# Optimization experiments

Measured on AMD Instinct MI355X. Metric: run time of the kernel, lower is better.

The kernel has to match this reference:

```python
import jax, jax.numpy as jnp
import numpy as np

N = 100000
E = 3200000
NEG_SLOPE = 0.2


def setup_inputs() -> dict:
    key = jax.random.key(0)
    ks = jax.random.split(key, 12)
    x = jax.random.normal(ks[0], (N, 4), dtype=jnp.float32)
    edge_index = jax.random.randint(ks[1], (2, E), 0, N, dtype=jnp.int64)
    # GATConv(4, 16, heads=4): lin (no bias), att_src/att_dst [H, C], bias [H*C]
    W1 = jax.random.normal(ks[2], (4, 4 * 16), dtype=jnp.float32) * 0.5
    as1 = jax.random.normal(ks[3], (4, 16), dtype=jnp.float32) * 0.5
    ad1 = jax.random.normal(ks[4], (4, 16), dtype=jnp.float32) * 0.5
    b1 = jnp.zeros((64,), dtype=jnp.float32)
    # GATConv(64, 2, heads=4)
    W2 = jax.random.normal(ks[5], (64, 4 * 2), dtype=jnp.float32) * 0.125
    as2 = jax.random.normal(ks[6], (4, 2), dtype=jnp.float32) * 0.5
    ad2 = jax.random.normal(ks[7], (4, 2), dtype=jnp.float32) * 0.5
    b2 = jnp.zeros((8,), dtype=jnp.float32)
    # out head Linear(8, 1)
    Wout = jax.random.normal(ks[8], (8, 1), dtype=jnp.float32) * 0.35
    bout = jnp.zeros((1,), dtype=jnp.float32)
    return {"x": x, "edge_index": edge_index, "W1": W1, "as1": as1, "ad1": ad1,
            "b1": b1, "W2": W2, "as2": as2, "ad2": ad2, "b2": b2,
            "Wout": Wout, "bout": bout}


def gat_conv(x, ei, W, a_src, a_dst, b, H, C, n):
    # PyG GATConv (concat=True, negative_slope=0.2), self-loops already in ei
    xw = (x @ W).reshape(n, H, C)                      # [N, H, C]
    src, dst = ei[0], ei[1]
    alpha_s = jnp.einsum('nhc,hc->nh', xw, a_src)      # [N, H]
    alpha_d = jnp.einsum('nhc,hc->nh', xw, a_dst)      # [N, H]
    e = jax.nn.leaky_relu(alpha_s[src] + alpha_d[dst], NEG_SLOPE)  # [E, H]
    # segment softmax over incoming edges of each destination node
    m = jax.ops.segment_max(e, dst, num_segments=n)    # [N, H]
    e = jnp.exp(e - m[dst])
    denom = jax.ops.segment_sum(e, dst, num_segments=n)
    alpha = e / (denom[dst] + 1e-16)                   # [E, H]
    msg = xw[src] * alpha[:, :, None]                  # [E, H, C]
    out = jax.ops.segment_sum(msg, dst, num_segments=n)  # [N, H, C]
    return out.reshape(n, H * C) + b


def reference(x, edge_index, W1, as1, ad1, b1, W2, as2, ad2, b2, Wout, bout):
    n = x.shape[0]
    ar = jnp.arange(n, dtype=edge_index.dtype)
    ei = jnp.concatenate([edge_index, jnp.stack([ar, ar])], axis=1)  # add self-loops
    h = jax.nn.elu(gat_conv(x, ei, W1, as1, ad1, b1, 4, 16, n))       # [N, 64]
    h = jax.nn.elu(gat_conv(h, ei, W2, as2, ad2, b2, 4, 2, n))        # [N, 8]
    g = jnp.mean(h, axis=0, keepdims=True)  # global_mean_pool, batch all zeros -> [1, 8]
    return jax.nn.sigmoid(g @ Wout + bout)  # [1, 1]
```

## Files before the change

kernel.cpp:

```cpp
#include <hip/hip_runtime.h>
#include <hip/hip_fp8.h>

#define NEG 0.2f
#define BSZ 224
#define MAXBUK 512
#define NBIN 512

typedef float v2f __attribute__((ext_vector_type(2)));

__device__ __forceinline__ float elufast(float x){ return x > 0.0f ? x : __expf(x) - 1.0f; }
__device__ __forceinline__ float b2f(unsigned short b){ return __uint_as_float((unsigned)b << 16); }
__device__ __forceinline__ unsigned short f2b(float x){
    unsigned u = __float_as_uint(x);
    return (unsigned short)((u + 0x7FFFu + ((u >> 16) & 1u)) >> 16);
}

__device__ __forceinline__ void fma8(uint2 r, float w, v2f* acc){
    v2f w2 = {w, w};
    v2f f0 = __builtin_amdgcn_cvt_pk_f32_fp8(r.x, false);
    v2f f1 = __builtin_amdgcn_cvt_pk_f32_fp8(r.x, true);
    v2f f2 = __builtin_amdgcn_cvt_pk_f32_fp8(r.y, false);
    v2f f3 = __builtin_amdgcn_cvt_pk_f32_fp8(r.y, true);
    acc[0] = __builtin_elementwise_fma(f0, w2, acc[0]);
    acc[1] = __builtin_elementwise_fma(f1, w2, acc[1]);
    acc[2] = __builtin_elementwise_fma(f2, w2, acc[2]);
    acc[3] = __builtin_elementwise_fma(f3, w2, acc[3]);
}

__global__ void k_l1_node(const float* __restrict__ x, const float* __restrict__ W1,
                          const float* __restrict__ as1, const float* __restrict__ ad1,
                          unsigned char* __restrict__ xw1, uint2* __restrict__ asvb,
                          float* __restrict__ adv, int N){
    __shared__ float sW[256], sA[64], sD[64];
    int tid = threadIdx.x;
    sW[tid] = W1[tid];
    if (tid < 64){ sA[tid] = as1[tid]; sD[tid] = ad1[tid]; }
    __syncthreads();
    int i = blockIdx.x * 256 + tid;
    if (i >= N) return;
    float4 xv = ((const float4*)x)[i];
    const v2f* sW0 = (const v2f*)sW;
    const v2f* sW1v = (const v2f*)(sW + 64);
    const v2f* sW2v = (const v2f*)(sW + 128);
    const v2f* sW3v = (const v2f*)(sW + 192);
    v2f xx = {xv.x, xv.x}, yy = {xv.y, xv.y}, zz = {xv.z, xv.z}, ww = {xv.w, xv.w};
    v2f xwv[32];
    #pragma unroll
    for (int j = 0; j < 32; j++){
        v2f t = xx * sW0[j];
        t = __builtin_elementwise_fma(yy, sW1v[j], t);
        t = __builtin_elementwise_fma(zz, sW2v[j], t);
        t = __builtin_elementwise_fma(ww, sW3v[j], t);
        xwv[j] = t;
    }
    unsigned wv[16];
    #pragma unroll
    for (int j = 0; j < 16; j++){
        unsigned p = 0;
        p = __builtin_amdgcn_cvt_pk_fp8_f32(xwv[2 * j].x,     xwv[2 * j].y,     p, false);
        p = __builtin_amdgcn_cvt_pk_fp8_f32(xwv[2 * j + 1].x, xwv[2 * j + 1].y, p, true);
        wv[j] = p;
    }
    uint4* dp = (uint4*)(xw1 + (size_t)i * 64);
    dp[0] = make_uint4(wv[0],  wv[1],  wv[2],  wv[3]);
    dp[1] = make_uint4(wv[4],  wv[5],  wv[6],  wv[7]);
    dp[2] = make_uint4(wv[8],  wv[9],  wv[10], wv[11]);
    dp[3] = make_uint4(wv[12], wv[13], wv[14], wv[15]);
    const v2f* sAv = (const v2f*)sA;
    const v2f* sDv = (const v2f*)sD;
    float al[4];
    #pragma unroll
    for (int h = 0; h < 4; h++){
        v2f asv = {0.f, 0.f}, adw = {0.f, 0.f};
        #pragma unroll
        for (int c2 = 0; c2 < 8; c2++){
            asv = __builtin_elementwise_fma(xwv[h * 8 + c2], sAv[h * 8 + c2], asv);
            adw = __builtin_elementwise_fma(xwv[h * 8 + c2], sDv[h * 8 + c2], adw);
        }
        al[h] = asv.x + asv.y;
        adv[i * 4 + h] = adw.x + adw.y;
    }
    asvb[i] = make_uint2((unsigned)f2b(al[0]) | ((unsigned)f2b(al[1]) << 16),
                         (unsigned)f2b(al[2]) | ((unsigned)f2b(al[3]) << 16));
}

__global__ void k_bcount(const int* __restrict__ dst, int* __restrict__ blkcnt,
                         int E, int chunksz, int nbuk){
    __shared__ int hist[MAXBUK];
    for (int b = threadIdx.x; b < nbuk; b += 256) hist[b] = 0;
    __syncthreads();
    int e0 = blockIdx.x * chunksz, e1 = min(E, e0 + chunksz);
    for (int e = e0 + threadIdx.x; e < e1; e += 256)
        atomicAdd(&hist[(unsigned)dst[e] / BSZ], 1);
    __syncthreads();
    for (int b = threadIdx.x; b < nbuk; b += 256)
        blkcnt[b * NBIN + blockIdx.x] = hist[b];
}

__global__ void k_scanA(int* __restrict__ blkcnt, int* __restrict__ btot){
    __shared__ int ts[256];
    int b = blockIdx.x, t = threadIdx.x;
    int base = b * NBIN + t * 2;
    int a0 = blkcnt[base], a1 = blkcnt[base + 1];
    int sum = a0 + a1;
    ts[t] = sum; __syncthreads();
    for (int s = 1; s < 256; s <<= 1){
        int tmp = (t >= s) ? ts[t - s] : 0;
        __syncthreads();
        ts[t] += tmp;
        __syncthreads();
    }
    int excl = ts[t] - sum;
    blkcnt[base] = excl;
    blkcnt[base + 1] = excl + a0;
    if (t == 255) btot[b] = ts[255];
}

__global__ void k_scanB(const int* __restrict__ btot, int* __restrict__ bstart, int nbuk){
    __shared__ int ts[512];
    int t = threadIdx.x;
    int v = (t < nbuk) ? btot[t] : 0;
    int orig = v;
    ts[t] = v; __syncthreads();
    for (int s = 1; s < 512; s <<= 1){
        int tmp = (t >= s) ? ts[t - s] : 0;
        __syncthreads();
        ts[t] += tmp;
        __syncthreads();
    }
    if (t < nbuk) bstart[t] = ts[t] - orig;
    if (t == 511) bstart[nbuk] = ts[511];
}

__global__ void k_bin(const int* __restrict__ src, const int* __restrict__ dst,
                      const int* __restrict__ blkcnt, const int* __restrict__ bstart,
                      unsigned* __restrict__ staged, int E, int chunksz, int nbuk){
    __shared__ int cur[MAXBUK];
    for (int b = threadIdx.x; b < nbuk; b += 256)
        cur[b] = bstart[b] + blkcnt[b * NBIN + blockIdx.x];
    __syncthreads();
    int e0 = blockIdx.x * chunksz, e1 = min(E, e0 + chunksz);
    for (int e = e0 + threadIdx.x; e < e1; e += 256){
        int d = dst[e];
        int buk = (unsigned)d / BSZ;
        int pos = atomicAdd(&cur[buk], 1);
        staged[pos] = (unsigned)src[e] | ((unsigned)(d - buk * BSZ) << 17);
    }
}

__global__ void k_local(const int* __restrict__ bstart, const unsigned* __restrict__ staged,
                        int* __restrict__ offp, int* __restrict__ csr, int N){
    __shared__ int deg[BSZ];
    __shared__ int cur[BSZ];
    __shared__ int ts[256];
    int b = blockIdx.x, t = threadIdx.x;
    int lo = b * BSZ, hi = min(N, lo + BSZ);
    int e0 = bstart[b], e1 = bstart[b + 1];
    if (t < BSZ) deg[t] = 0;
    __syncthreads();
    for (int e = e0 + t; e < e1; e += 256)
        atomicAdd(&deg[staged[e] >> 17], 1);
    __syncthreads();
    int v = (t < BSZ) ? deg[t] : 0;
    ts[t] = v; __syncthreads();
    for (int s = 1; s < 256; s <<= 1){
        int tmp = (t >= s) ? ts[t - s] : 0;
        __syncthreads();
        ts[t] += tmp;
        __syncthreads();
    }
    if (t < BSZ){
        cur[t] = e0 + ts[t] - v;
        if (lo + t < hi) offp[lo + t] = e0 + ts[t];
    }
    __syncthreads();
    for (int e = e0 + t; e < e1; e += 256){
        unsigned se = staged[e];
        int pos = atomicAdd(&cur[se >> 17], 1);
        csr[pos] = (int)(se & 0x1FFFFu);
    }
}

__global__ void k_l1_gather(const int* __restrict__ off, const int* __restrict__ csr,
                            const uint2* __restrict__ asvb, const float* __restrict__ adv,
                            const unsigned char* __restrict__ xw1, const float* __restrict__ b1,
                            unsigned char* __restrict__ h1f8, int N){
    int tid = threadIdx.x;
    int wid = (int)(((long)blockIdx.x * 256 + tid) >> 6);
    if (wid >= N) return;
    int lane = tid & 63;
    int g = lane >> 3;
    int q = lane & 7;
    int h = q >> 1;
    float advd = adv[wid * 4 + h];
    const unsigned char* xwq = xw1 + q * 8;
    const char* asvbh = (const char*)asvb + h * 2;

    v2f acc2[4] = {{0.f, 0.f}, {0.f, 0.f}, {0.f, 0.f}, {0.f, 0.f}};
    float den = 0.f;
    int k = wid ? off[wid - 1] : 0;
    int end = off[wid];
    for (; k + 32 <= end; k += 32){
        int s0 = csr[k + g];
        int s1 = csr[k + 8 + g];
        int s2 = csr[k + 16 + g];
        int s3 = csr[k + 24 + g];
        uint2 r0 = *(const uint2*)(xwq + ((size_t)s0 << 6));
        uint2 r1 = *(const uint2*)(xwq + ((size_t)s1 << 6));
        uint2 r2 = *(const uint2*)(xwq + ((size_t)s2 << 6));
        uint2 r3 = *(const uint2*)(xwq + ((size_t)s3 << 6));
        float a0 = b2f(*(const unsigned short*)(asvbh + ((size_t)s0 << 3)));
        float a1 = b2f(*(const unsigned short*)(asvbh + ((size_t)s1 << 3)));
        float a2 = b2f(*(const unsigned short*)(asvbh + ((size_t)s2 << 3)));
        float a3 = b2f(*(const unsigned short*)(asvbh + ((size_t)s3 << 3)));
        float t0 = a0 + advd, t1 = a1 + advd, t2 = a2 + advd, t3 = a3 + advd;
        float w0 = __expf(fmaxf(t0, NEG * t0));
        float w1 = __expf(fmaxf(t1, NEG * t1));
        float w2 = __expf(fmaxf(t2, NEG * t2));
        float w3 = __expf(fmaxf(t3, NEG * t3));
        den += (w0 + w1) + (w2 + w3);
        fma8(r0, w0, acc2);
        fma8(r1, w1, acc2);
        fma8(r2, w2, acc2);
        fma8(r3, w3, acc2);
    }
    if (k + 16 <= end){
        int sA = csr[k + g];
        int sB = csr[k + 8 + g];
        uint2 rA = *(const uint2*)(xwq + ((size_t)sA << 6));
        uint2 rB = *(const uint2*)(xwq + ((size_t)sB << 6));
        float aA = b2f(*(const unsigned short*)(asvbh + ((size_t)sA << 3)));
        float aB = b2f(*(const unsigned short*)(asvbh + ((size_t)sB << 3)));
        float tA = aA + advd, tB = aB + advd;
        float wA = __expf(fmaxf(tA, NEG * tA));
        float wB = __expf(fmaxf(tB, NEG * tB));
        den += wA + wB;
        fma8(rA, wA, acc2);
        fma8(rB, wB, acc2);
        k += 16;
    }
    for (; k < end; k += 8){
        int e = k + g;
        bool valid = e < end;
        int s = csr[valid ? e : end - 1];
        uint2 r = *(const uint2*)(xwq + ((size_t)s << 6));
        float a = b2f(*(const unsigned short*)(asvbh + ((size_t)s << 3)));
        float t = a + advd;
        float w = valid ? __expf(fmaxf(t, NEG * t)) : 0.f;
        den += w;
        fma8(r, w, acc2);
    }

    v2f t0, t1, t2, t3;
    t0.x = __shfl_xor(acc2[0].x, 32); t0.y = __shfl_xor(acc2[0].y, 32);
    t1.x = __shfl_xor(acc2[1].x, 32); t1.y = __shfl_xor(acc2[1].y, 32);
    t2.x = __shfl_xor(acc2[2].x, 32); t2.y = __shfl_xor(acc2[2].y, 32);
    t3.x = __shfl_xor(acc2[3].x, 32); t3.y = __shfl_xor(acc2[3].y, 32);
    bool gb2 = (lane & 32) != 0;
    v2f n0 = gb2 ? (acc2[2] + t2) : (acc2[0] + t0);
    v2f n1 = gb2 ? (acc2[3] + t3) : (acc2[1] + t1);
    v2f u0, u1;
    u0.x = __shfl_xor(n0.x, 16); u0.y = __shfl_xor(n0.y, 16);
    u1.x = __shfl_xor(n1.x, 16); u1.y = __shfl_xor(n1.y, 16);
    bool gb1 = (lane & 16) != 0;
    v2f rr = gb1 ? (n1 + u1) : (n0 + u0);
    v2f z;
    z.x = __shfl_xor(rr.x, 8); z.y = __shfl_xor(rr.y, 8);
    rr += z;
    bool gb0 = (lane & 8) != 0;
    den += __shfl_xor(den, 8);
    den += __shfl_xor(den, 16);
    den += __shfl_xor(den, 32);
    float val = gb0 ? rr.y : rr.x;

    int c = q * 8 + g;
    float aself = b2f(*(const unsigned short*)(asvbh + ((size_t)wid << 3)));
    float tsv = aself + advd;
    float ws = __expf(fmaxf(tsv, NEG * tsv));
    unsigned selfb = xw1[(size_t)wid * 64 + c];
    v2f sf = __builtin_amdgcn_cvt_pk_f32_fp8(selfb, false);
    float asel = val + ws * sf.x;
    float inv = 1.0f / (den + ws + 1e-16f);
    float o = elufast(asel * inv + b1[c]);
    unsigned p = __builtin_amdgcn_cvt_pk_fp8_f32(o, o, 0, false);
    h1f8[(size_t)wid * 64 + c] = (unsigned char)p;
}

__global__ void k_l2_node(const unsigned char* __restrict__ h1f8, const float* __restrict__ W2,
                          const float* __restrict__ ad2, float* __restrict__ xw2,
                          float* __restrict__ adv2, int N){
    __shared__ float sW[512], sD[8];
    int tid = threadIdx.x;
    sW[tid] = W2[tid];
    sW[256 + tid] = W2[256 + tid];
    if (tid < 8) sD[tid] = ad2[tid];
    __syncthreads();
    int i = blockIdx.x * 256 + tid;
    if (i >= N) return;
    const uint2* rp = (const uint2*)(h1f8 + (size_t)i * 64);
    v2f acc2[4] = {{0.f, 0.f}, {0.f, 0.f}, {0.f, 0.f}, {0.f, 0.f}};
    #pragma unroll
    for (int b8 = 0; b8 < 8; b8++){
        uint2 r = rp[b8];
        v2f f0 = __builtin_amdgcn_cvt_pk_f32_fp8(r.x, false);
        v2f f1 = __builtin_amdgcn_cvt_pk_f32_fp8(r.x, true);
        v2f f2 = __builtin_amdgcn_cvt_pk_f32_fp8(r.y, false);
        v2f f3 = __builtin_amdgcn_cvt_pk_f32_fp8(r.y, true);
        float f[8] = {f0.x, f0.y, f1.x, f1.y, f2.x, f2.y, f3.x, f3.y};
        #pragma unroll
        for (int j = 0; j < 8; j++){
            v2f hcv = {f[j], f[j]};
            const v2f* wrow = (const v2f*)&sW[(b8 * 8 + j) * 8];
            acc2[0] = __builtin_elementwise_fma(hcv, wrow[0], acc2[0]);
            acc2[1] = __builtin_elementwise_fma(hcv, wrow[1], acc2[1]);
            acc2[2] = __builtin_elementwise_fma(hcv, wrow[2], acc2[2]);
            acc2[3] = __builtin_elementwise_fma(hcv, wrow[3], acc2[3]);
        }
    }
    float4* xo = (float4*)(xw2 + (size_t)i * 8);
    xo[0] = make_float4(acc2[0].x, acc2[0].y, acc2[1].x, acc2[1].y);
    xo[1] = make_float4(acc2[2].x, acc2[2].y, acc2[3].x, acc2[3].y);
    float4 dv;
    dv.x = acc2[0].x * sD[0] + acc2[0].y * sD[1];
    dv.y = acc2[1].x * sD[2] + acc2[1].y * sD[3];
    dv.z = acc2[2].x * sD[4] + acc2[2].y * sD[5];
    dv.w = acc2[3].x * sD[6] + acc2[3].y * sD[7];
    *(float4*)(adv2 + (size_t)i * 4) = dv;
}

__global__ void k_l2_gather(const int* __restrict__ off, const int* __restrict__ csr,
                            const float* __restrict__ adv2, const float* __restrict__ xw2,
                            const float* __restrict__ b2, const float* __restrict__ as2,
                            float* __restrict__ pool, int N){
    __shared__ float lpool[8];
    int tid = threadIdx.x;
    if (tid < 8) lpool[tid] = 0.f;
    __syncthreads();
    int wid = (int)(((long)blockIdx.x * 256 + tid) >> 6);
    if (wid < N){
        int lane = tid & 63;
        int g = lane >> 2;
        int hh = lane & 3;
        float2 a2h = *(const float2*)&as2[hh * 2];
        float advd = adv2[wid * 4 + hh];
        const char* xwh = (const char*)xw2 + hh * 8;
        v2f accv = {0.f, 0.f};
        float den = 0.f;

        auto edge = [&](int s, bool valid){
            v2f v = *(const v2f*)(xwh + ((size_t)s << 5));
            float al = v.x * a2h.x + v.y * a2h.y;
            float t = al + advd;
            float w = valid ? __expf(fmaxf(t, NEG * t)) : 0.f;
            den += w;
            v2f w2 = {w, w};
            accv = __builtin_elementwise_fma(v, w2, accv);
        };

        int k = wid ? off[wid - 1] : 0;
        int end = off[wid];
        for (; k + 32 <= end; k += 32){
            int s0 = csr[k + g], s1 = csr[k + 16 + g];
            edge(s0, true); edge(s1, true);
        }
        for (; k < end; k += 16){
            int e = k + g;
            bool valid = e < end;
            int s = csr[valid ? e : end - 1];
            edge(s, valid);
        }
        #pragma unroll
        for (int m = 4; m <= 32; m <<= 1){
            accv.x += __shfl_xor(accv.x, m);
            accv.y += __shfl_xor(accv.y, m);
            den    += __shfl_xor(den, m);
        }
        if (g == 0){
            v2f v = *(const v2f*)(xwh + ((size_t)wid << 5));
            float al = v.x * a2h.x + v.y * a2h.y;
            float t = al + advd;
            float ws = __expf(fmaxf(t, NEG * t));
            den += ws;
            accv.x += ws * v.x;
            accv.y += ws * v.y;
            float inv = 1.0f / (den + 1e-16f);
            float o0 = elufast(accv.x * inv + b2[hh * 2]);
            float o1 = elufast(accv.y * inv + b2[hh * 2 + 1]);
            atomicAdd(&lpool[hh * 2], o0);
            atomicAdd(&lpool[hh * 2 + 1], o1);
        }
    }
    __syncthreads();
    if (tid < 8) atomicAdd(&pool[(blockIdx.x & 63) * 8 + tid], lpool[tid]);
}

__global__ void k_final(const float* __restrict__ pool, const float* __restrict__ Wout,
                        const float* __restrict__ bout, float* __restrict__ out, float invN){
    int lane = threadIdx.x;
    const float4* p4 = (const float4*)(pool + lane * 8);
    float4 a = p4[0], b = p4[1];
    float v[8] = {a.x, a.y, a.z, a.w, b.x, b.y, b.z, b.w};
    #pragma unroll
    for (int m = 1; m <= 32; m <<= 1){
        #pragma unroll
        for (int j = 0; j < 8; j++) v[j] += __shfl_xor(v[j], m);
    }
    if (lane == 0){
        float z = bout[0];
        #pragma unroll
        for (int j = 0; j < 8; j++) z += v[j] * invN * Wout[j];
        out[0] = 1.0f / (1.0f + __expf(-z));
    }
}

extern "C" void kernel_launch(void* const* d_in, const int* in_sizes, int n_in,
                              void* d_out, int out_size, void* d_ws, size_t ws_size,
                              hipStream_t stream){
    const float* x    = (const float*)d_in[0];
    const int*   ei   = (const int*)d_in[1];
    const float* W1   = (const float*)d_in[2];
    const float* as1  = (const float*)d_in[3];
    const float* ad1  = (const float*)d_in[4];
    const float* b1   = (const float*)d_in[5];
    const float* W2   = (const float*)d_in[6];
    const float* as2  = (const float*)d_in[7];
    const float* ad2  = (const float*)d_in[8];
    const float* b2   = (const float*)d_in[9];
    const float* Wout = (const float*)d_in[10];
    const float* bout = (const float*)d_in[11];
    float* out = (float*)d_out;

    int N = in_sizes[0] / 4;
    int E = in_sizes[1] / 2;
    const int* src = ei;
    const int* dst = ei + E;

    char* ws = (char*)d_ws;
    size_t off_b = 0;
    auto alloc = [&](size_t bytes)->void*{
        void* p = ws + off_b;
        off_b += (bytes + 255) & ~(size_t)255;
        return p;
    };
    unsigned char* xw1  = (unsigned char*)alloc((size_t)N * 64);
    unsigned char* h1f8 = (unsigned char*)alloc((size_t)N * 64);
    uint2*    asvb   = (uint2*)alloc((size_t)N * 8);
    float*    adv    = (float*)alloc((size_t)N * 4 * 4);
    float*    adv2   = (float*)alloc((size_t)N * 4 * 4);
    int*      blkcnt = (int*)alloc((size_t)MAXBUK * NBIN * 4);
    int*      btot   = (int*)alloc((size_t)MAXBUK * 4);
    int*      bstart = (int*)alloc((size_t)(MAXBUK + 1) * 4);
    unsigned* staged = (unsigned*)alloc((size_t)E * 4);
    int*      offp   = (int*)alloc((size_t)N * 4);
    int*      csr    = (int*)alloc((size_t)E * 4);
    float*    xw2    = (float*)alloc((size_t)N * 8 * 4);
    float*    pool   = (float*)alloc(64 * 8 * 4);

    int nbuk = (N + BSZ - 1) / BSZ;
    int chunksz = (E + NBIN - 1) / NBIN;

    hipMemsetAsync(pool, 0, 64 * 8 * 4, stream);

    k_bcount<<<NBIN, 256, 0, stream>>>(dst, blkcnt, E, chunksz, nbuk);
    k_l1_node<<<(N + 255) / 256, 256, 0, stream>>>(x, W1, as1, ad1, xw1, asvb, adv, N);
    k_scanA<<<nbuk, 256, 0, stream>>>(blkcnt, btot);
    k_scanB<<<1, 512, 0, stream>>>(btot, bstart, nbuk);
    k_bin<<<NBIN, 256, 0, stream>>>(src, dst, blkcnt, bstart, staged, E, chunksz, nbuk);
    k_local<<<nbuk, 256, 0, stream>>>(bstart, staged, offp, csr, N);

    k_l1_gather<<<(int)(((long)N * 64 + 255) / 256), 256, 0, stream>>>(
        offp, csr, asvb, adv, xw1, b1, h1f8, N);
    k_l2_node<<<(N + 255) / 256, 256, 0, stream>>>(h1f8, W2, ad2, xw2, adv2, N);
    k_l2_gather<<<(int)(((long)N * 64 + 255) / 256), 256, 0, stream>>>(
        offp, csr, adv2, xw2, b2, as2, pool, N);
    k_final<<<1, 64, 0, stream>>>(pool, Wout, bout, out, 1.0f / (float)N);
}
```

Before: 187.3 us.

## Build CSR with fixed-capacity buckets and global atomics, dropping scan kernels

```diff
diff --git a/kernel.cpp b/kernel.cpp
--- a/kernel.cpp
+++ b/kernel.cpp
@@ -5,6 +5,7 @@
 #define BSZ 224
 #define MAXBUK 512
 #define NBIN 512
+#define CAP 16384
 
 typedef float v2f __attribute__((ext_vector_type(2)));
 
@@ -84,63 +85,22 @@
                          (unsigned)f2b(al[2]) | ((unsigned)f2b(al[3]) << 16));
 }
 
-__global__ void k_bcount(const int* __restrict__ dst, int* __restrict__ blkcnt,
-                         int E, int chunksz, int nbuk){
+__global__ void k_bin2(const int* __restrict__ src, const int* __restrict__ dst,
+                       int* __restrict__ gcnt, unsigned* __restrict__ staged,
+                       int E, int chunksz, int nbuk){
     __shared__ int hist[MAXBUK];
-    for (int b = threadIdx.x; b < nbuk; b += 256) hist[b] = 0;
+    __shared__ int cur[MAXBUK];
+    int tid = threadIdx.x;
+    for (int b = tid; b < nbuk; b += 256) hist[b] = 0;
     __syncthreads();
     int e0 = blockIdx.x * chunksz, e1 = min(E, e0 + chunksz);
-    for (int e = e0 + threadIdx.x; e < e1; e += 256)
+    for (int e = e0 + tid; e < e1; e += 256)
         atomicAdd(&hist[(unsigned)dst[e] / BSZ], 1);
     __syncthreads();
-    for (int b = threadIdx.x; b < nbuk; b += 256)
-        blkcnt[b * NBIN + blockIdx.x] = hist[b];
-}
-
-__global__ void k_scanA(int* __restrict__ blkcnt, int* __restrict__ btot){
-    __shared__ int ts[256];
-    int b = blockIdx.x, t = threadIdx.x;
-    int base = b * NBIN + t * 2;
-    int a0 = blkcnt[base], a1 = blkcnt[base + 1];
-    int sum = a0 + a1;
-    ts[t] = sum; __syncthreads();
-    for (int s = 1; s < 256; s <<= 1){
-        int tmp = (t >= s) ? ts[t - s] : 0;
-        __syncthreads();
-        ts[t] += tmp;
-        __syncthreads();
-    }
-    int excl = ts[t] - sum;
-    blkcnt[base] = excl;
-    blkcnt[base + 1] = excl + a0;
-    if (t == 255) btot[b] = ts[255];
-}
-
-__global__ void k_scanB(const int* __restrict__ btot, int* __restrict__ bstart, int nbuk){
-    __shared__ int ts[512];
-    int t = threadIdx.x;
-    int v = (t < nbuk) ? btot[t] : 0;
-    int orig = v;
-    ts[t] = v; __syncthreads();
-    for (int s = 1; s < 512; s <<= 1){
-        int tmp = (t >= s) ? ts[t - s] : 0;
-        __syncthreads();
-        ts[t] += tmp;
-        __syncthreads();
-    }
-    if (t < nbuk) bstart[t] = ts[t] - orig;
-    if (t == 511) bstart[nbuk] = ts[511];
-}
-
-__global__ void k_bin(const int* __restrict__ src, const int* __restrict__ dst,
-                      const int* __restrict__ blkcnt, const int* __restrict__ bstart,
-                      unsigned* __restrict__ staged, int E, int chunksz, int nbuk){
-    __shared__ int cur[MAXBUK];
-    for (int b = threadIdx.x; b < nbuk; b += 256)
-        cur[b] = bstart[b] + blkcnt[b * NBIN + blockIdx.x];
-    __syncthreads();
-    int e0 = blockIdx.x * chunksz, e1 = min(E, e0 + chunksz);
-    for (int e = e0 + threadIdx.x; e < e1; e += 256){
+    for (int b = tid; b < nbuk; b += 256)
+        cur[b] = b * CAP + atomicAdd(&gcnt[b], hist[b]);
+    __syncthreads();
+    for (int e = e0 + tid; e < e1; e += 256){
         int d = dst[e];
         int buk = (unsigned)d / BSZ;
         int pos = atomicAdd(&cur[buk], 1);
@@ -148,14 +108,14 @@
     }
 }
 
-__global__ void k_local(const int* __restrict__ bstart, const unsigned* __restrict__ staged,
-                        int* __restrict__ offp, int* __restrict__ csr, int N){
+__global__ void k_local(const unsigned* __restrict__ staged, const int* __restrict__ gcnt,
+                        int2* __restrict__ offp, int* __restrict__ csr, int N){
     __shared__ int deg[BSZ];
     __shared__ int cur[BSZ];
     __shared__ int ts[256];
     int b = blockIdx.x, t = threadIdx.x;
     int lo = b * BSZ, hi = min(N, lo + BSZ);
-    int e0 = bstart[b], e1 = bstart[b + 1];
+    int e0 = b * CAP, e1 = e0 + gcnt[b];
     if (t < BSZ) deg[t] = 0;
     __syncthreads();
     for (int e = e0 + t; e < e1; e += 256)
@@ -171,7 +131,7 @@
     }
     if (t < BSZ){
         cur[t] = e0 + ts[t] - v;
-        if (lo + t < hi) offp[lo + t] = e0 + ts[t];
+        if (lo + t < hi) offp[lo + t] = make_int2(e0 + ts[t] - v, e0 + ts[t]);
     }
     __syncthreads();
     for (int e = e0 + t; e < e1; e += 256){
@@ -181,7 +141,7 @@
     }
 }
 
-__global__ void k_l1_gather(const int* __restrict__ off, const int* __restrict__ csr,
+__global__ void k_l1_gather(const int2* __restrict__ offp, const int* __restrict__ csr,
                             const uint2* __restrict__ asvb, const float* __restrict__ adv,
                             const unsigned char* __restrict__ xw1, const float* __restrict__ b1,
                             unsigned char* __restrict__ h1f8, int N){
@@ -198,8 +158,8 @@
 
     v2f acc2[4] = {{0.f, 0.f}, {0.f, 0.f}, {0.f, 0.f}, {0.f, 0.f}};
     float den = 0.f;
-    int k = wid ? off[wid - 1] : 0;
-    int end = off[wid];
+    int2 rng = offp[wid];
+    int k = rng.x, end = rng.y;
     for (; k + 32 <= end; k += 32){
         int s0 = csr[k + g];
         int s1 = csr[k + 8 + g];
@@ -328,7 +288,7 @@
     *(float4*)(adv2 + (size_t)i * 4) = dv;
 }
 
-__global__ void k_l2_gather(const int* __restrict__ off, const int* __restrict__ csr,
+__global__ void k_l2_gather(const int2* __restrict__ offp, const int* __restrict__ csr,
                             const float* __restrict__ adv2, const float* __restrict__ xw2,
                             const float* __restrict__ b2, const float* __restrict__ as2,
                             float* __restrict__ pool, int N){
@@ -357,8 +317,8 @@
             accv = __builtin_elementwise_fma(v, w2, accv);
         };
 
-        int k = wid ? off[wid - 1] : 0;
-        int end = off[wid];
+        int2 rng = offp[wid];
+        int k = rng.x, end = rng.y;
         for (; k + 32 <= end; k += 32){
             int s0 = csr[k + g], s1 = csr[k + 16 + g];
             edge(s0, true); edge(s1, true);
@@ -447,12 +407,10 @@
     uint2*    asvb   = (uint2*)alloc((size_t)N * 8);
     float*    adv    = (float*)alloc((size_t)N * 4 * 4);
     float*    adv2   = (float*)alloc((size_t)N * 4 * 4);
-    int*      blkcnt = (int*)alloc((size_t)MAXBUK * NBIN * 4);
-    int*      btot   = (int*)alloc((size_t)MAXBUK * 4);
-    int*      bstart = (int*)alloc((size_t)(MAXBUK + 1) * 4);
-    unsigned* staged = (unsigned*)alloc((size_t)E * 4);
-    int*      offp   = (int*)alloc((size_t)N * 4);
-    int*      csr    = (int*)alloc((size_t)E * 4);
+    int*      gcnt   = (int*)alloc((size_t)MAXBUK * 4);
+    unsigned* staged = (unsigned*)alloc((size_t)MAXBUK * CAP * 4);
+    int2*     offp   = (int2*)alloc((size_t)N * 8);
+    int*      csr    = (int*)alloc((size_t)MAXBUK * CAP * 4);
     float*    xw2    = (float*)alloc((size_t)N * 8 * 4);
     float*    pool   = (float*)alloc(64 * 8 * 4);
 
@@ -460,13 +418,11 @@
     int chunksz = (E + NBIN - 1) / NBIN;
 
     hipMemsetAsync(pool, 0, 64 * 8 * 4, stream);
-
-    k_bcount<<<NBIN, 256, 0, stream>>>(dst, blkcnt, E, chunksz, nbuk);
+    hipMemsetAsync(gcnt, 0, (size_t)MAXBUK * 4, stream);
+
+    k_bin2<<<NBIN, 256, 0, stream>>>(src, dst, gcnt, staged, E, chunksz, nbuk);
     k_l1_node<<<(N + 255) / 256, 256, 0, stream>>>(x, W1, as1, ad1, xw1, asvb, adv, N);
-    k_scanA<<<nbuk, 256, 0, stream>>>(blkcnt, btot);
-    k_scanB<<<1, 512, 0, stream>>>(btot, bstart, nbuk);
-    k_bin<<<NBIN, 256, 0, stream>>>(src, dst, blkcnt, bstart, staged, E, chunksz, nbuk);
-    k_local<<<nbuk, 256, 0, stream>>>(bstart, staged, offp, csr, N);
+    k_local<<<nbuk, 256, 0, stream>>>(staged, gcnt, offp, csr, N);
 
     k_l1_gather<<<(int)(((long)N * 64 + 255) / 256), 256, 0, stream>>>(
         offp, csr, asvb, adv, xw1, b1, h1f8, N);
```

Result: slower. 191.1 us (+2.1%).
